# Performance work log

Hardware: AMD Instinct MI355X
Metric: run time of the kernel (lower is better)

The kernel has to match this reference:

```python
import jax, jax.numpy as jnp
import numpy as np

B, DIN, D, C = 8192, 1024, 768, 16384

def setup_inputs() -> dict:
    key = jax.random.key(0)
    k1, k2, k3 = jax.random.split(key, 3)
    x = jax.random.normal(k1, (B, DIN), dtype=jnp.float32)
    W = jax.random.normal(k2, (DIN, D), dtype=jnp.float32) * 0.02  # backbone final projection
    centroids = jax.random.normal(k3, (C, D), dtype=jnp.float32)
    return {"x": x, "W": W, "centroids": centroids}

def reference(x, W, centroids):
    # backbone embedding: [B, D]
    e = x @ W
    # -||e - c||^2 via algebraic expansion: ||e||^2 + ||c||^2 - 2 e.c
    # (same math as -((e[:,None]-centroids[None])**2).sum(-1), GEMM-formulated)
    e_sq = jnp.sum(e * e, axis=-1, keepdims=True)          # [B, 1]
    c_sq = jnp.sum(centroids * centroids, axis=-1)         # [C]
    cross = e @ centroids.T                                # [B, C]
    return -(e_sq + c_sq[None, :] - 2.0 * cross)           # [B, C]
```

## Files before the change

kernel.cpp:

```cpp
#include <hip/hip_runtime.h>
#include <hip/hip_bf16.h>
#include <cstdint>
#include <cstddef>

#define BB   8192
#define DIN  1024
#define DD   768
#define CC   16384

typedef __bf16 bf16x8 __attribute__((ext_vector_type(8)));
typedef __bf16 bf16x4 __attribute__((ext_vector_type(4)));
typedef float  floatx4 __attribute__((ext_vector_type(4)));

__device__ __forceinline__ void gload_lds16(const void* g, void* l) {
    __builtin_amdgcn_global_load_lds(
        (const __attribute__((address_space(1))) void*)g,
        (__attribute__((address_space(3))) void*)l,
        16, 0, 0);
}


__global__ __launch_bounds__(256) void f2b_kernel(const float4* __restrict__ in,
                                                  bf16x4* __restrict__ out) {
    size_t i = (size_t)blockIdx.x * 256 + threadIdx.x;
    float4 v = in[i];
    bf16x4 o;
    o.x = (__bf16)v.x; o.y = (__bf16)v.y; o.z = (__bf16)v.z; o.w = (__bf16)v.w;
    out[i] = o;
}

__global__ __launch_bounds__(256) void row_convert_sumsq_f32(const float* __restrict__ src,
                                                             __bf16* __restrict__ dst,
                                                             float* __restrict__ sq,
                                                             int Dd) {
    int row = blockIdx.x;
    int tid = threadIdx.x, lane = tid & 63, wave = tid >> 6;
    const float* s = src + (size_t)row * Dd;
    __bf16* d = dst + (size_t)row * Dd;
    float acc = 0.f;
    for (int j = tid; j < Dd; j += 256) {
        __bf16 b = (__bf16)s[j];
        d[j] = b;
        float f = (float)b;
        acc += f * f;
    }
    for (int off = 32; off > 0; off >>= 1) acc += __shfl_xor(acc, off, 64);
    __shared__ float red[4];
    if (lane == 0) red[wave] = acc;
    __syncthreads();
    if (tid == 0) sq[row] = red[0] + red[1] + red[2] + red[3];
}

__global__ __launch_bounds__(256) void row_sumsq_bf16(const __bf16* __restrict__ src,
                                                      float* __restrict__ sq,
                                                      int Dd) {
    int row = blockIdx.x;
    int tid = threadIdx.x, lane = tid & 63, wave = tid >> 6;
    const __bf16* s = src + (size_t)row * Dd;
    float acc = 0.f;
    for (int j = tid; j < Dd; j += 256) {
        float f = (float)s[j];
        acc += f * f;
    }
    for (int off = 32; off > 0; off >>= 1) acc += __shfl_xor(acc, off, 64);
    __shared__ float red[4];
    if (lane == 0) red[wave] = acc;
    __syncthreads();
    if (tid == 0) sq[row] = red[0] + red[1] + red[2] + red[3];
}

__global__ __launch_bounds__(256) void transpose_w(const float* __restrict__ W,
                                                   __bf16* __restrict__ Wt,
                                                   int K, int N) {
    __shared__ float tile[32][33];
    int bx = blockIdx.x * 32;
    int by = blockIdx.y * 32;
    int tx = threadIdx.x & 31, ty = threadIdx.x >> 5;
    for (int i = 0; i < 32; i += 8)
        tile[ty + i][tx] = W[(size_t)(by + ty + i) * N + bx + tx];
    __syncthreads();
    for (int i = 0; i < 32; i += 8)
        Wt[(size_t)(bx + ty + i) * K + by + tx] = (__bf16)tile[tx][ty + i];
}

template <int EPI, int SWIZ>
__global__ __launch_bounds__(256) void gemm_bt(const __bf16* __restrict__ A,
                                               const __bf16* __restrict__ Bt,
                                               void* __restrict__ OutP,
                                               const float* __restrict__ esq,
                                               const float* __restrict__ csq,
                                               int M, int N, int K) {
    __shared__ __bf16 As[128 * 64];
    __shared__ __bf16 Bs[128 * 64];
    const int tid  = threadIdx.x;
    const int lane = tid & 63;
    const int wave = tid >> 6;

    int bm, bn;
    if (SWIZ == 1) {
        int flat = blockIdx.x;
        int xcd = flat & 7;
        int j = flat >> 3;
        bn = (xcd * 16 + (j & 15)) * 128;
        bm = (j >> 4) * 128;
    } else {
        int flat = blockIdx.x;
        int nt = N / 128;
        bm = (flat / nt) * 128;
        bn = (flat % nt) * 128;
    }

    floatx4 acc[4][4] = {};

    const int srow = lane >> 3;
    const int sc   = ((lane & 7) ^ srow) * 8;

    const int wm   = (wave & 1) * 64;
    const int wn   = (wave >> 1) * 64;
    const int frow = lane & 15;
    const int quad = lane >> 4;
    const int swz  = frow & 7;

    for (int k0 = 0; k0 < K; k0 += 64) {
        __syncthreads();
        #pragma unroll
        for (int i = 0; i < 4; ++i) {
            int row = wave * 32 + i * 8;
            const __bf16* ga = A  + (size_t)(bm + row + srow) * K + k0 + sc;
            gload_lds16(ga, &As[(size_t)row * 64]);
            const __bf16* gb = Bt + (size_t)(bn + row + srow) * K + k0 + sc;
            gload_lds16(gb, &Bs[(size_t)row * 64]);
        }
        asm volatile("s_waitcnt vmcnt(0)" ::: "memory");
        __syncthreads();

        #pragma unroll
        for (int kb = 0; kb < 2; ++kb) {
            bf16x8 af[4], bfr[4];
            #pragma unroll
            for (int mi = 0; mi < 4; ++mi)
                af[mi] = *(const bf16x8*)&As[(wm + mi * 16 + frow) * 64 +
                                             (((kb * 4 + quad) ^ swz) * 8)];
            #pragma unroll
            for (int ni = 0; ni < 4; ++ni)
                bfr[ni] = *(const bf16x8*)&Bs[(wn + ni * 16 + frow) * 64 +
                                              (((kb * 4 + quad) ^ swz) * 8)];
            #pragma unroll
            for (int mi = 0; mi < 4; ++mi)
                #pragma unroll
                for (int ni = 0; ni < 4; ++ni)
                    acc[mi][ni] = __builtin_amdgcn_mfma_f32_16x16x32_bf16(
                        bfr[ni], af[mi], acc[mi][ni], 0, 0, 0);
        }
    }

    const int mrow = lane & 15;
    const int nq   = (lane >> 4) * 4;
    if (EPI == 1) {
        float* Out = (float*)OutP;
        #pragma unroll
        for (int mi = 0; mi < 4; ++mi) {
            int row = bm + wm + mi * 16 + mrow;
            float es = esq[row];
            size_t rb = (size_t)row * N;
            #pragma unroll
            for (int ni = 0; ni < 4; ++ni) {
                int col = bn + wn + ni * 16 + nq;
                floatx4 cs = *(const floatx4*)&csq[col];
                floatx4 a = acc[mi][ni];
                floatx4 v;
                #pragma unroll
                for (int r = 0; r < 4; ++r)
                    v[r] = 2.0f * a[r] - es - cs[r];
                __builtin_nontemporal_store(v, (floatx4*)&Out[rb + col]);
            }
        }
    } else {
        __bf16* Out = (__bf16*)OutP;
        #pragma unroll
        for (int mi = 0; mi < 4; ++mi) {
            int row = bm + wm + mi * 16 + mrow;
            size_t rb = (size_t)row * N;
            #pragma unroll
            for (int ni = 0; ni < 4; ++ni) {
                int col = bn + wn + ni * 16 + nq;
                floatx4 a = acc[mi][ni];
                bf16x4 o;
                #pragma unroll
                for (int r = 0; r < 4; ++r) o[r] = (__bf16)a[r];
                *(bf16x4*)&Out[rb + col] = o;
            }
        }
    }
}


extern "C" void kernel_launch(void* const* d_in, const int* in_sizes, int n_in,
                              void* d_out, int out_size, void* d_ws, size_t ws_size,
                              hipStream_t stream) {
    const float* x    = (const float*)d_in[0];
    const float* W    = (const float*)d_in[1];
    const float* cent = (const float*)d_in[2];
    float* out = (float*)d_out;

    char* ws = (char*)d_ws;
    __bf16* xb  = (__bf16*)ws;  ws += (size_t)BB * DIN * 2;
    __bf16* Wt  = (__bf16*)ws;  ws += (size_t)DD * DIN * 2;
    __bf16* cb  = (__bf16*)ws;  ws += (size_t)CC * DD * 2;
    float*  csq = (float*)ws;   ws += (size_t)CC * 4;
    __bf16* eb  = (__bf16*)ws;  ws += (size_t)BB * DD * 2;
    float*  esq = (float*)ws;   ws += (size_t)BB * 4;

    f2b_kernel<<<(BB * DIN) / (256 * 4), 256, 0, stream>>>((const float4*)x, (bf16x4*)xb);
    transpose_w<<<dim3(DD / 32, DIN / 32), 256, 0, stream>>>(W, Wt, DIN, DD);
    row_convert_sumsq_f32<<<CC, 256, 0, stream>>>(cent, cb, csq, DD);
    gemm_bt<0, 0><<<(BB / 128) * (DD / 128), 256, 0, stream>>>(xb, Wt, eb, nullptr, nullptr,
                                                               BB, DD, DIN);
    row_sumsq_bf16<<<BB, 256, 0, stream>>>(eb, esq, DD);
    gemm_bt<1, 1><<<(BB / 128) * (CC / 128), 256, 0, stream>>>(eb, cb, out, esq, csq,
                                                               BB, CC, DD);
}
```

Baseline: 830.0 us.

## Add double-buffered 256x256 tile GEMM for the distance stage

Replaces the 128x128 single-buffered GEMM used for the large e·c^T product with a new 512-thread kernel that computes 256x256 tiles and double-buffers LDS. Global-to-LDS loads for the next k-tile are spread across four compute phases, with MFMA priority raised, so memory traffic overlaps with matrix math. Larger tiles raise arithmetic intensity and cut redundant operand loads. In exchange the kernel uses 128KB of LDS and many accumulator registers, which limits occupancy, and it launches fewer blocks.

```diff
diff --git a/kernel.cpp b/kernel.cpp
--- a/kernel.cpp
+++ b/kernel.cpp
@@ -83,12 +83,10 @@
         Wt[(size_t)(bx + ty + i) * K + by + tx] = (__bf16)tile[tx][ty + i];
 }
 
-template <int EPI, int SWIZ>
+template <int EPI>
 __global__ __launch_bounds__(256) void gemm_bt(const __bf16* __restrict__ A,
                                                const __bf16* __restrict__ Bt,
                                                void* __restrict__ OutP,
-                                               const float* __restrict__ esq,
-                                               const float* __restrict__ csq,
                                                int M, int N, int K) {
     __shared__ __bf16 As[128 * 64];
     __shared__ __bf16 Bs[128 * 64];
@@ -96,19 +94,10 @@
     const int lane = tid & 63;
     const int wave = tid >> 6;
 
-    int bm, bn;
-    if (SWIZ == 1) {
-        int flat = blockIdx.x;
-        int xcd = flat & 7;
-        int j = flat >> 3;
-        bn = (xcd * 16 + (j & 15)) * 128;
-        bm = (j >> 4) * 128;
-    } else {
-        int flat = blockIdx.x;
-        int nt = N / 128;
-        bm = (flat / nt) * 128;
-        bn = (flat % nt) * 128;
-    }
+    int flat = blockIdx.x;
+    int ntn = N / 128;
+    int bm = (flat / ntn) * 128;
+    int bn = (flat % ntn) * 128;
 
     floatx4 acc[4][4] = {};
 
@@ -156,16 +145,162 @@
 
     const int mrow = lane & 15;
     const int nq   = (lane >> 4) * 4;
+    __bf16* Out = (__bf16*)OutP;
+    #pragma unroll
+    for (int mi = 0; mi < 4; ++mi) {
+        int row = bm + wm + mi * 16 + mrow;
+        size_t rb = (size_t)row * N;
+        #pragma unroll
+        for (int ni = 0; ni < 4; ++ni) {
+            int col = bn + wn + ni * 16 + nq;
+            floatx4 a = acc[mi][ni];
+            bf16x4 o;
+            #pragma unroll
+            for (int r = 0; r < 4; ++r) o[r] = (__bf16)a[r];
+            *(bf16x4*)&Out[rb + col] = o;
+        }
+    }
+}
+
+template <int EPI>
+__global__ __launch_bounds__(512, 2) void gemm256(const __bf16* __restrict__ A,
+                                                  const __bf16* __restrict__ Bt,
+                                                  void* __restrict__ OutP,
+                                                  const float* __restrict__ esq,
+                                                  const float* __restrict__ csq,
+                                                  int M, int N, int K) {
+    __shared__ __bf16 As[2][256 * 64];
+    __shared__ __bf16 Bs[2][256 * 64];
+
+    const int tid  = threadIdx.x;
+    const int lane = tid & 63;
+    const int wave = tid >> 6;
+    const int wr   = wave >> 2;
+    const int wc   = wave & 3;
+
+    int bm, bn;
+    {
+        int flat = blockIdx.x;
+        int ntn = N >> 8;
+        if ((ntn & 7) == 0) {
+            int xcd = flat & 7, j = flat >> 3;
+            int spx = ntn >> 3;
+            bn = (xcd * spx + (j % spx)) << 8;
+            bm = (j / spx) << 8;
+        } else {
+            bm = (flat / ntn) << 8;
+            bn = (flat % ntn) << 8;
+        }
+    }
+
+    const __bf16* Ablk = A  + (size_t)bm * K;
+    const __bf16* Bblk = Bt + (size_t)bn * K;
+
+    const int srow = lane >> 3;
+    const int sc   = ((lane & 7) ^ srow) << 3;
+    const int frow = lane & 15;
+    const int quad = lane >> 4;
+    const int swz  = frow & 7;
+
+    floatx4 acc[8][4] = {};
+    bf16x8 bfr[4][2];
+    const int nt = K >> 6;
+
+#define STAGE_A(BUF, T, H) { \
+    const int r0_ = (H) * 128 + wave * 8; \
+    const __bf16* g_ = Ablk + (size_t)(r0_ + srow) * K + ((T) << 6) + sc; \
+    gload_lds16(g_, &As[BUF][r0_ * 64]); \
+    gload_lds16(g_ + (size_t)64 * K, &As[BUF][(r0_ + 64) * 64]); \
+}
+#define STAGE_B(BUF, T, H) { \
+    const int r0_ = (H) * 128 + wave * 8; \
+    const __bf16* g_ = Bblk + (size_t)(r0_ + srow) * K + ((T) << 6) + sc; \
+    gload_lds16(g_, &Bs[BUF][r0_ * 64]); \
+    gload_lds16(g_ + (size_t)64 * K, &Bs[BUF][(r0_ + 64) * 64]); \
+}
+
+    STAGE_B(0, 0, 0)
+    STAGE_B(0, 0, 1)
+    STAGE_A(0, 0, 0)
+    STAGE_A(0, 0, 1)
+    if (nt > 1) {
+        STAGE_B(1, 1, 0)
+        STAGE_B(1, 1, 1)
+        asm volatile("s_waitcnt vmcnt(4)" ::: "memory");
+    } else {
+        asm volatile("s_waitcnt vmcnt(0)" ::: "memory");
+    }
+    __builtin_amdgcn_s_barrier();
+
+#define PHASE(MB, STAGE_STMT, DO_LDB) { \
+    bf16x8 af[2][2]; \
+    { \
+        const __bf16* ap_ = Ac + (size_t)(wr * 128 + (MB) * 16 + frow) * 64; \
+        af[0][0] = *(const bf16x8*)(ap_ + ((quad ^ swz) << 3)); \
+        af[0][1] = *(const bf16x8*)(ap_ + (((4 + quad) ^ swz) << 3)); \
+        af[1][0] = *(const bf16x8*)(ap_ + 16 * 64 + ((quad ^ swz) << 3)); \
+        af[1][1] = *(const bf16x8*)(ap_ + 16 * 64 + (((4 + quad) ^ swz) << 3)); \
+    } \
+    if (DO_LDB) { \
+        const __bf16* bp_ = Bc + (size_t)(wc * 64 + frow) * 64; \
+        _Pragma("unroll") \
+        for (int ni = 0; ni < 4; ++ni) { \
+            bfr[ni][0] = *(const bf16x8*)(bp_ + ni * 16 * 64 + ((quad ^ swz) << 3)); \
+            bfr[ni][1] = *(const bf16x8*)(bp_ + ni * 16 * 64 + (((4 + quad) ^ swz) << 3)); \
+        } \
+    } \
+    STAGE_STMT; \
+    __builtin_amdgcn_s_barrier(); \
+    asm volatile("s_waitcnt lgkmcnt(0)" ::: "memory"); \
+    __builtin_amdgcn_s_setprio(1); \
+    _Pragma("unroll") \
+    for (int ni = 0; ni < 4; ++ni) { \
+        acc[(MB)][ni]     = __builtin_amdgcn_mfma_f32_16x16x32_bf16(bfr[ni][0], af[0][0], acc[(MB)][ni], 0, 0, 0); \
+        acc[(MB)][ni]     = __builtin_amdgcn_mfma_f32_16x16x32_bf16(bfr[ni][1], af[0][1], acc[(MB)][ni], 0, 0, 0); \
+        acc[(MB) + 1][ni] = __builtin_amdgcn_mfma_f32_16x16x32_bf16(bfr[ni][0], af[1][0], acc[(MB) + 1][ni], 0, 0, 0); \
+        acc[(MB) + 1][ni] = __builtin_amdgcn_mfma_f32_16x16x32_bf16(bfr[ni][1], af[1][1], acc[(MB) + 1][ni], 0, 0, 0); \
+    } \
+    __builtin_amdgcn_s_setprio(0); \
+}
+
+    for (int t = 0; t < nt; ++t) {
+        const int cur = t & 1;
+        const __bf16* Ac = As[cur];
+        const __bf16* Bc = Bs[cur];
+        const bool pA = (t + 1 < nt);
+        const bool pB = (t + 2 < nt);
+
+        PHASE(0, if (pA) STAGE_A(cur ^ 1, t + 1, 0), 1)
+        __builtin_amdgcn_s_barrier();
+        PHASE(2, if (pA) STAGE_A(cur ^ 1, t + 1, 1), 0)
+        __builtin_amdgcn_s_barrier();
+        PHASE(4, if (pB) STAGE_B(cur, t + 2, 0), 0)
+        __builtin_amdgcn_s_barrier();
+        PHASE(6, if (pB) STAGE_B(cur, t + 2, 1), 0)
+        if (pB) {
+            asm volatile("s_waitcnt vmcnt(4)" ::: "memory");
+        } else {
+            asm volatile("s_waitcnt vmcnt(0)" ::: "memory");
+        }
+        __builtin_amdgcn_s_barrier();
+    }
+
+#undef PHASE
+#undef STAGE_A
+#undef STAGE_B
+
+    const int mrow = lane & 15;
+    const int nq   = (lane >> 4) << 2;
     if (EPI == 1) {
         float* Out = (float*)OutP;
         #pragma unroll
-        for (int mi = 0; mi < 4; ++mi) {
-            int row = bm + wm + mi * 16 + mrow;
+        for (int mi = 0; mi < 8; ++mi) {
+            int row = bm + wr * 128 + mi * 16 + mrow;
             float es = esq[row];
             size_t rb = (size_t)row * N;
             #pragma unroll
             for (int ni = 0; ni < 4; ++ni) {
-                int col = bn + wn + ni * 16 + nq;
+                int col = bn + wc * 64 + ni * 16 + nq;
                 floatx4 cs = *(const floatx4*)&csq[col];
                 floatx4 a = acc[mi][ni];
                 floatx4 v;
@@ -178,12 +313,12 @@
     } else {
         __bf16* Out = (__bf16*)OutP;
         #pragma unroll
-        for (int mi = 0; mi < 4; ++mi) {
-            int row = bm + wm + mi * 16 + mrow;
+        for (int mi = 0; mi < 8; ++mi) {
+            int row = bm + wr * 128 + mi * 16 + mrow;
             size_t rb = (size_t)row * N;
             #pragma unroll
             for (int ni = 0; ni < 4; ++ni) {
-                int col = bn + wn + ni * 16 + nq;
+                int col = bn + wc * 64 + ni * 16 + nq;
                 floatx4 a = acc[mi][ni];
                 bf16x4 o;
                 #pragma unroll
@@ -214,9 +349,8 @@
     f2b_kernel<<<(BB * DIN) / (256 * 4), 256, 0, stream>>>((const float4*)x, (bf16x4*)xb);
     transpose_w<<<dim3(DD / 32, DIN / 32), 256, 0, stream>>>(W, Wt, DIN, DD);
     row_convert_sumsq_f32<<<CC, 256, 0, stream>>>(cent, cb, csq, DD);
-    gemm_bt<0, 0><<<(BB / 128) * (DD / 128), 256, 0, stream>>>(xb, Wt, eb, nullptr, nullptr,
-                                                               BB, DD, DIN);
+    gemm_bt<0><<<(BB / 128) * (DD / 128), 256, 0, stream>>>(xb, Wt, eb, BB, DD, DIN);
     row_sumsq_bf16<<<BB, 256, 0, stream>>>(eb, esq, DD);
-    gemm_bt<1, 1><<<(BB / 128) * (CC / 128), 256, 0, stream>>>(eb, cb, out, esq, csq,
-                                                               BB, CC, DD);
-}
+    gemm256<1><<<(BB / 256) * (CC / 256), 512, 0, stream>>>(eb, cb, out, esq, csq,
+                                                            BB, CC, DD);
+}
```

After: 836.6 us. No clear change (+0.8%).
